# Kernel tuning notes

Measured on AMD Instinct MI355X. Metric: run time of the kernel, lower is better.

Reference implementation:

```python
import jax, jax.numpy as jnp
import numpy as np

EPS = 1e-5
NUM_HEADS = 16


def layernorm(x, g, b):
    m = jnp.mean(x, axis=-1, keepdims=True)
    v = jnp.mean(jnp.square(x - m), axis=-1, keepdims=True)
    return (x - m) * jax.lax.rsqrt(v + EPS) * g + b


def setup_inputs() -> dict:
    key = jax.random.key(0)
    ks = jax.random.split(key, 8)
    B, S, E, F = 16, 512, 1024, 4096
    s_e = 1.0 / np.sqrt(E)
    s_f = 1.0 / np.sqrt(F)
    return {
        "input": jax.random.normal(ks[0], (B, S, E), jnp.float32),
        "ln1_g": jnp.ones((E,), jnp.float32),
        "ln1_b": jnp.zeros((E,), jnp.float32),
        "wq": jax.random.normal(ks[1], (E, E), jnp.float32) * s_e,
        "bq": jnp.zeros((E,), jnp.float32),
        "wk": jax.random.normal(ks[2], (E, E), jnp.float32) * s_e,
        "bk": jnp.zeros((E,), jnp.float32),
        "wv": jax.random.normal(ks[3], (E, E), jnp.float32) * s_e,
        "bv": jnp.zeros((E,), jnp.float32),
        "wo": jax.random.normal(ks[4], (E, E), jnp.float32) * s_e,
        "bo": jnp.zeros((E,), jnp.float32),
        "ln2_g": jnp.ones((E,), jnp.float32),
        "ln2_b": jnp.zeros((E,), jnp.float32),
        "w1": jax.random.normal(ks[5], (E, F), jnp.float32) * s_e,
        "b1": jnp.zeros((F,), jnp.float32),
        "w2": jax.random.normal(ks[6], (F, E), jnp.float32) * s_f,
        "b2": jnp.zeros((E,), jnp.float32),
    }


def attention(x, wq, bq, wk, bk, wv, bv, wo, bo):
    B, S, E = x.shape
    H = NUM_HEADS
    D = E // H
    q = (x @ wq + bq).reshape(B, S, H, D)
    k = (x @ wk + bk).reshape(B, S, H, D)
    v = (x @ wv + bv).reshape(B, S, H, D)
    scores = jnp.einsum("bqhd,bkhd->bhqk", q, k) * (1.0 / np.sqrt(D))
    attn = jax.nn.softmax(scores, axis=-1)
    out = jnp.einsum("bhqk,bkhd->bqhd", attn, v).reshape(B, S, E)
    return out @ wo + bo


def reference(input, ln1_g, ln1_b, wq, bq, wk, bk, wv, bv, wo, bo,
              ln2_g, ln2_b, w1, b1, w2, b2):
    # pre-LN attention + residual
    x = layernorm(input, ln1_g, ln1_b)
    x = attention(x, wq, bq, wk, bk, wv, bv, wo, bo)
    x = x + input
    # pre-LN MLP (GELU exact, matching nn.GELU default) + residual
    y = layernorm(x, ln2_g, ln2_b)
    y = jax.nn.gelu(y @ w1 + b1, approximate=False)
    y = y @ w2 + b2
    return x + y
```

## Files before the change

### kernel.cpp

```cpp
#include <hip/hip_runtime.h>
#include <hip/hip_bf16.h>


typedef __bf16 bf16x8 __attribute__((ext_vector_type(8)));
typedef __bf16 bf16x4 __attribute__((ext_vector_type(4)));
typedef float  f32x4  __attribute__((ext_vector_type(4)));

#define EPI_QKV  0
#define EPI_RES  1
#define EPI_GELU 2

__device__ __forceinline__ void async_copy16(const void* g, void* l) {
  __builtin_amdgcn_global_load_lds((const __attribute__((address_space(1))) void*)g,
                                   (__attribute__((address_space(3))) void*)l, 16, 0, 0);
}

__global__ __launch_bounds__(256) void prep_weights(
    const float* __restrict__ wq, const float* __restrict__ wk,
    const float* __restrict__ wv, const float* __restrict__ wo,
    const float* __restrict__ w1, const float* __restrict__ w2,
    const float* __restrict__ bq, const float* __restrict__ bk,
    const float* __restrict__ bv,
    __bf16* __restrict__ wqkvT, __bf16* __restrict__ woT,
    __bf16* __restrict__ w1T, __bf16* __restrict__ w2T, float* __restrict__ bqkv) {
  const int bid = blockIdx.x;
  if (bid >= 12288) {
    const int i = (bid - 12288) * 256 + threadIdx.x;
    bqkv[i] = (i < 1024) ? bq[i] : ((i < 2048) ? bk[i - 1024] : bv[i - 2048]);
    return;
  }
  const float* in;
  __bf16* out;
  int K, N, tile;
  if (bid < 4096) {
    const int w = bid >> 10;
    tile = bid & 1023;
    in = (w == 0) ? wq : (w == 1) ? wk : (w == 2) ? wv : wo;
    out = (w == 3) ? woT : (wqkvT + (size_t)w * 1024 * 1024);
    K = 1024; N = 1024;
  } else if (bid < 8192) { tile = bid - 4096; in = w1; out = w1T; K = 1024; N = 4096; }
  else                   { tile = bid - 8192; in = w2; out = w2T; K = 4096; N = 1024; }
  const int ntx = N >> 5;
  const int bx = tile % ntx, by = tile / ntx;
  const int n0 = bx * 32, k0 = by * 32;

  __shared__ float tilebuf[32][33];
  const int tx = threadIdx.x & 31, ty = threadIdx.x >> 5;
#pragma unroll
  for (int i = 0; i < 4; i++)
    tilebuf[ty + i * 8][tx] = in[(size_t)(k0 + ty + i * 8) * N + n0 + tx];
  __syncthreads();
#pragma unroll
  for (int i = 0; i < 4; i++)
    out[(size_t)(n0 + ty + i * 8) * K + k0 + tx] = (__bf16)tilebuf[tx][ty + i * 8];
}

__device__ __forceinline__ float block_sum(float v, float* red) {
#pragma unroll
  for (int off = 32; off; off >>= 1) v += __shfl_down(v, off);
  const int w = threadIdx.x >> 6;
  __syncthreads();
  if ((threadIdx.x & 63) == 0) red[w] = v;
  __syncthreads();
  return red[0] + red[1] + red[2] + red[3];
}

__global__ __launch_bounds__(256) void ln_kernel(const float* __restrict__ x,
                                                 const float* __restrict__ g,
                                                 const float* __restrict__ bta,
                                                 __bf16* __restrict__ out) {
  __shared__ float red[8];
  const int row = blockIdx.x, t = threadIdx.x;
  const float4 v = ((const float4*)(x + (size_t)row * 1024))[t];
  float s = v.x + v.y + v.z + v.w;
  s = block_sum(s, red);
  const float mean = s * (1.0f / 1024.0f);
  const float d0 = v.x - mean, d1 = v.y - mean, d2 = v.z - mean, d3 = v.w - mean;
  float vs = d0 * d0 + d1 * d1 + d2 * d2 + d3 * d3;
  vs = block_sum(vs, red);
  const float rstd = rsqrtf(vs * (1.0f / 1024.0f) + 1e-5f);
  const float4 gg = ((const float4*)g)[t];
  const float4 bb = ((const float4*)bta)[t];
  bf16x4 o;
  o[0] = (__bf16)(d0 * rstd * gg.x + bb.x);
  o[1] = (__bf16)(d1 * rstd * gg.y + bb.y);
  o[2] = (__bf16)(d2 * rstd * gg.z + bb.z);
  o[3] = (__bf16)(d3 * rstd * gg.w + bb.w);
  ((bf16x4*)out)[(size_t)row * 256 + t] = o;
}

template <int EPI>
__global__ __launch_bounds__(256, 2) void gemm_bt(const __bf16* __restrict__ A,
                                                  const __bf16* __restrict__ Bt,
                                                  const float* __restrict__ bias,
                                                  const float* __restrict__ res,
                                                  void* __restrict__ out,
                                                  void* __restrict__ out2,
                                                  int N, int K) {
  __shared__ __bf16 lA[128 * 64];
  __shared__ __bf16 lB[128 * 64];
  const int t = threadIdx.x;
  const int wave = t >> 6, lane = t & 63;
  const int lm = lane & 15, lq = lane >> 4;

  const int Ntiles = gridDim.x;
  const int flat = blockIdx.y * Ntiles + blockIdx.x;
  const int xcd = flat & 7;
  const int local = flat >> 3;
  const int tn = local % Ntiles;
  const int tm = (local / Ntiles) * 8 + xcd;
  const int m0 = tm * 128, n0 = tn * 128;
  const int wm = (wave & 1) * 64, wn = (wave >> 1) * 64;

  f32x4 acc[4][4] = {};

  const int srow = t >> 3, sslot = t & 7;
  const int schunk = sslot ^ (srow & 7);
  const __bf16* aSrc = A + (size_t)(m0 + srow) * K + schunk * 8;
  const __bf16* bSrc = Bt + (size_t)(n0 + srow) * K + schunk * 8;

  for (int k0 = 0; k0 < K; k0 += 64) {
#pragma unroll
    for (int i = 0; i < 4; i++) {
      async_copy16(aSrc + (size_t)(i * 32) * K, lA + i * 2048 + t * 8);
      async_copy16(bSrc + (size_t)(i * 32) * K, lB + i * 2048 + t * 8);
    }
    aSrc += 64; bSrc += 64;
    __syncthreads();
#pragma unroll
    for (int kk = 0; kk < 2; kk++) {
      bf16x8 af[4], bf[4];
      const int slot = (kk * 4 + lq) ^ (lm & 7);
#pragma unroll
      for (int i = 0; i < 4; i++) {
        af[i] = *(const bf16x8*)&lA[(wm + i * 16 + lm) * 64 + slot * 8];
        bf[i] = *(const bf16x8*)&lB[(wn + i * 16 + lm) * 64 + slot * 8];
      }
#pragma unroll
      for (int mi = 0; mi < 4; mi++)
#pragma unroll
        for (int ni = 0; ni < 4; ni++)
          acc[mi][ni] = __builtin_amdgcn_mfma_f32_16x16x32_bf16(af[mi], bf[ni], acc[mi][ni], 0, 0, 0);
    }
    __syncthreads();
  }

#pragma unroll
  for (int mi = 0; mi < 4; mi++) {
    const int gr = m0 + wm + mi * 16 + lq * 4;
#pragma unroll
    for (int ni = 0; ni < 4; ni++) {
      const int gc = n0 + wn + ni * 16 + lm;
      const float bv = bias[gc];
#pragma unroll
      for (int r = 0; r < 4; r++) {
        float v = acc[mi][ni][r] + bv;
        const int row = gr + r;
        if (EPI == EPI_GELU) {
          v = 0.5f * v * (1.0f + erff(v * 0.70710678118654752f));
          ((__bf16*)out)[(size_t)row * N + gc] = (__bf16)v;
        } else if (EPI == EPI_RES) {
          ((float*)out)[(size_t)row * N + gc] = v + res[(size_t)row * N + gc];
        } else {
          if (gc < 2048) {
            ((__bf16*)out)[(size_t)row * 2048 + gc] = (__bf16)v;
          } else {
            const int d = gc & 63, hh = (gc - 2048) >> 6;
            const int bb = row >> 9, ss = row & 511;
            ((__bf16*)out2)[(((size_t)bb * 16 + hh) * 64 + d) * 512 + ss] = (__bf16)v;
          }
        }
      }
    }
  }
}

__global__ __launch_bounds__(256) void attn_kernel(const __bf16* __restrict__ qk,
                                                   const __bf16* __restrict__ Vt,
                                                   __bf16* __restrict__ outA) {
  __shared__ __bf16 lK[128 * 64];
  __shared__ __bf16 lV[64 * 128];
  __shared__ __bf16 lP[4][16 * 128];
  const int t = threadIdx.x, wave = t >> 6, lane = t & 63;
  const int lm = lane & 15, lq = lane >> 4;
  const int sw = lm & 7;
  const int flat = blockIdx.x;
  const int xcd = flat & 7, local = flat >> 3;
  const int qt = local & 7;
  const int bh = (local >> 3) * 8 + xcd;
  const int h = bh & 15, b = bh >> 4;
  const int q0 = qt * 64 + wave * 16;

  const size_t qrow = (size_t)(b * 512 + q0 + lm) * 2048 + h * 64;
  bf16x8 aq0 = *(const bf16x8*)&qk[qrow + lq * 8];
  bf16x8 aq1 = *(const bf16x8*)&qk[qrow + 32 + lq * 8];

  float mrow[4] = {-3e38f, -3e38f, -3e38f, -3e38f};
  float lrow[4] = {0.f, 0.f, 0.f, 0.f};
  f32x4 o[4] = {};

  const int krow = t >> 3;
  const int kchunk = (t & 7) ^ (krow & 7);
  const __bf16* kSrc = qk + (size_t)(b * 512 + krow) * 2048 + 1024 + h * 64 + kchunk * 8;
  const int vrow = t >> 4;
  const int vchunk = (t & 15) ^ (vrow & 7);
  const __bf16* vSrc = Vt + ((size_t)bh * 64 + vrow) * 512 + vchunk * 8;

  for (int kt = 0; kt < 4; kt++) {
#pragma unroll
    for (int i = 0; i < 4; i++) {
      async_copy16(kSrc + (size_t)(kt * 128 + i * 32) * 2048, lK + i * 2048 + t * 8);
      async_copy16(vSrc + kt * 128 + (size_t)(i * 16) * 512, lV + i * 2048 + t * 8);
    }
    __syncthreads();

    f32x4 s[8];
#pragma unroll
    for (int ni = 0; ni < 8; ni++) {
      bf16x8 bk0 = *(const bf16x8*)&lK[(ni * 16 + lm) * 64 + ((lq ^ sw) * 8)];
      bf16x8 bk1 = *(const bf16x8*)&lK[(ni * 16 + lm) * 64 + (((4 + lq) ^ sw) * 8)];
      f32x4 z = {};
      z = __builtin_amdgcn_mfma_f32_16x16x32_bf16(aq0, bk0, z, 0, 0, 0);
      z = __builtin_amdgcn_mfma_f32_16x16x32_bf16(aq1, bk1, z, 0, 0, 0);
      s[ni] = z;
    }
#pragma unroll
    for (int ni = 0; ni < 8; ni++)
#pragma unroll
      for (int r = 0; r < 4; r++) s[ni][r] *= 0.125f;

    float mnew[4], alpha[4];
#pragma unroll
    for (int r = 0; r < 4; r++) {
      float mx = s[0][r];
#pragma unroll
      for (int ni = 1; ni < 8; ni++) mx = fmaxf(mx, s[ni][r]);
#pragma unroll
      for (int off = 1; off < 16; off <<= 1) mx = fmaxf(mx, __shfl_xor(mx, off));
      mnew[r] = fmaxf(mrow[r], mx);
      alpha[r] = __expf(mrow[r] - mnew[r]);
      mrow[r] = mnew[r];
    }
    float rs[4] = {0.f, 0.f, 0.f, 0.f};
#pragma unroll
    for (int ni = 0; ni < 8; ni++)
#pragma unroll
      for (int r = 0; r < 4; r++) {
        const float p = __expf(s[ni][r] - mnew[r]);
        s[ni][r] = p;
        rs[r] += p;
      }
#pragma unroll
    for (int r = 0; r < 4; r++) {
#pragma unroll
      for (int off = 1; off < 16; off <<= 1) rs[r] += __shfl_xor(rs[r], off);
      lrow[r] = lrow[r] * alpha[r] + rs[r];
    }

#pragma unroll
    for (int ni = 0; ni < 8; ni++) {
      const int chunk = ni * 2 + (lm >> 3);
#pragma unroll
      for (int r = 0; r < 4; r++) {
        const int q = lq * 4 + r;
        lP[wave][q * 128 + ((chunk ^ (q & 7)) * 8) + (lm & 7)] = (__bf16)s[ni][r];
      }
    }
    asm volatile("s_waitcnt lgkmcnt(0)" ::: "memory");
    bf16x8 ap[4];
#pragma unroll
    for (int kc = 0; kc < 4; kc++)
      ap[kc] = *(const bf16x8*)&lP[wave][lm * 128 + (((kc * 4 + lq) ^ sw) * 8)];

#pragma unroll
    for (int di = 0; di < 4; di++)
#pragma unroll
      for (int r = 0; r < 4; r++) o[di][r] *= alpha[r];

#pragma unroll
    for (int di = 0; di < 4; di++) {
#pragma unroll
      for (int kc = 0; kc < 4; kc++) {
        bf16x8 bv = *(const bf16x8*)&lV[(di * 16 + lm) * 128 + (((kc * 4 + lq) ^ sw) * 8)];
        o[di] = __builtin_amdgcn_mfma_f32_16x16x32_bf16(ap[kc], bv, o[di], 0, 0, 0);
      }
    }
    __syncthreads();
  }

#pragma unroll
  for (int di = 0; di < 4; di++)
#pragma unroll
    for (int r = 0; r < 4; r++) {
      const float v = o[di][r] / lrow[r];
      outA[(size_t)(b * 512 + q0 + lq * 4 + r) * 1024 + h * 64 + di * 16 + lm] = (__bf16)v;
    }
}

extern "C" void kernel_launch(void* const* d_in, const int* in_sizes, int n_in,
                              void* d_out, int out_size, void* d_ws, size_t ws_size,
                              hipStream_t stream) {
  const float* input = (const float*)d_in[0];
  const float* ln1_g = (const float*)d_in[1];
  const float* ln1_b = (const float*)d_in[2];
  const float* wq = (const float*)d_in[3];
  const float* bq = (const float*)d_in[4];
  const float* wk = (const float*)d_in[5];
  const float* bk = (const float*)d_in[6];
  const float* wv = (const float*)d_in[7];
  const float* bv = (const float*)d_in[8];
  const float* wo = (const float*)d_in[9];
  const float* bo = (const float*)d_in[10];
  const float* ln2_g = (const float*)d_in[11];
  const float* ln2_b = (const float*)d_in[12];
  const float* w1 = (const float*)d_in[13];
  const float* b1 = (const float*)d_in[14];
  const float* w2 = (const float*)d_in[15];
  const float* b2 = (const float*)d_in[16];

  char* ws = (char*)d_ws;
  __bf16* wqkvT = (__bf16*)(ws + 0);
  __bf16* woT   = (__bf16*)(ws + ((size_t)6 << 20));
  __bf16* w1T   = (__bf16*)(ws + ((size_t)8 << 20));
  __bf16* w2T   = (__bf16*)(ws + ((size_t)16 << 20));
  __bf16* qkbuf = (__bf16*)(ws + ((size_t)24 << 20));
  __bf16* vtbuf = (__bf16*)(ws + ((size_t)56 << 20));
  __bf16* abuf  = (__bf16*)(ws + ((size_t)72 << 20));
  float*  xbuf  = (float*) (ws + ((size_t)24 << 20));
  __bf16* ylnbuf= (__bf16*)(ws + ((size_t)56 << 20));
  __bf16* hbuf  = (__bf16*)(ws + ((size_t)72 << 20));
  float*  bqkv  = (float*) (ws + ((size_t)136 << 20));

  const dim3 blk(256);
  prep_weights<<<12300, blk, 0, stream>>>(wq, wk, wv, wo, w1, w2, bq, bk, bv,
                                          wqkvT, woT, w1T, w2T, bqkv);

  ln_kernel<<<8192, blk, 0, stream>>>(input, ln1_g, ln1_b, abuf);
  gemm_bt<EPI_QKV><<<dim3(24, 64), blk, 0, stream>>>(abuf, wqkvT, bqkv, nullptr,
                                                     qkbuf, vtbuf, 3072, 1024);
  attn_kernel<<<2048, blk, 0, stream>>>(qkbuf, vtbuf, abuf);
  gemm_bt<EPI_RES><<<dim3(8, 64), blk, 0, stream>>>(abuf, woT, bo, input,
                                                    xbuf, nullptr, 1024, 1024);
  ln_kernel<<<8192, blk, 0, stream>>>(xbuf, ln2_g, ln2_b, ylnbuf);
  gemm_bt<EPI_GELU><<<dim3(32, 64), blk, 0, stream>>>(ylnbuf, w1T, b1, nullptr,
                                                      hbuf, nullptr, 4096, 1024);
  gemm_bt<EPI_RES><<<dim3(8, 64), blk, 0, stream>>>(hbuf, w2T, b2, xbuf,
                                                    d_out, nullptr, 1024, 4096);
}
```

Measured before the change: 484.1 us.

## Add 256x256-tile 8-wave GEMM with interleaved staging for QKV and FC1

Adds a new GEMM kernel using 512-thread blocks and 256x256 output tiles. It double-buffers LDS and splits each K-step into four MFMA quads, with asynchronous global-to-LDS loads interleaved between them and wave priority raised around the MFMAs. The QKV projection and the first MLP GEMM now use this kernel. The aim is more data reuse per tile and better overlap of loads with matrix math, at the cost of heavy register and LDS use (128 KB LDS, large accumulator arrays) and fewer blocks per grid.

```diff
diff --git a/kernel.cpp b/kernel.cpp
--- a/kernel.cpp
+++ b/kernel.cpp
@@ -175,6 +175,159 @@
   }
 }
 
+#define MFMA_QUAD(MI0)                                                         \
+  do {                                                                         \
+    _Pragma("unroll") for (int kk = 0; kk < 2; ++kk) {                         \
+      _Pragma("unroll") for (int ni = 0; ni < 4; ++ni) {                       \
+        acc[MI0][ni] = __builtin_amdgcn_mfma_f32_16x16x32_bf16(                \
+            af[MI0][kk], bf[ni][kk], acc[MI0][ni], 0, 0, 0);                   \
+        acc[(MI0) + 1][ni] = __builtin_amdgcn_mfma_f32_16x16x32_bf16(          \
+            af[(MI0) + 1][kk], bf[ni][kk], acc[(MI0) + 1][ni], 0, 0, 0);       \
+      }                                                                        \
+    }                                                                          \
+  } while (0)
+
+#define READ_A(MI)                                                             \
+  _Pragma("unroll") for (int kk = 0; kk < 2; ++kk)                             \
+      af[MI][kk] = *(const bf16x8*)&bufA[(wm * 128 + (MI)*16 + lm) * 64 +      \
+                                         (((kk * 4 + lq) ^ sw) * 8)];
+
+template <int EPI>
+__global__ __launch_bounds__(512, 2) void gemm8_bt(const __bf16* __restrict__ A,
+                                                   const __bf16* __restrict__ Bt,
+                                                   const float* __restrict__ bias,
+                                                   void* __restrict__ out,
+                                                   void* __restrict__ out2,
+                                                   int N, int K) {
+  __shared__ __bf16 lA[2 * 256 * 64];
+  __shared__ __bf16 lB[2 * 256 * 64];
+  const int t = threadIdx.x;
+  const int wave = t >> 6, lane = t & 63;
+  const int lm = lane & 15, lq = lane >> 4, sw = lm & 7;
+  const int wm = wave >> 2, wn = wave & 3;
+
+  const int Ntiles = gridDim.x;
+  const int flat = blockIdx.y * Ntiles + blockIdx.x;
+  const int xcd = flat & 7;
+  const int local = flat >> 3;
+  const int tn = local % Ntiles;
+  const int tm = (local / Ntiles) * 8 + xcd;
+  const int m0 = tm * 256, n0 = tn * 256;
+
+  const int NT = K >> 6;
+
+  const int srow = t >> 3;
+  const int schunk = (t & 7) ^ (srow & 7);
+  const __bf16* aBase = A + (size_t)(m0 + srow) * K + schunk * 8;
+  const __bf16* bBase = Bt + (size_t)(n0 + srow) * K + schunk * 8;
+  __bf16* ldA = lA + t * 8;
+  __bf16* ldB = lB + t * 8;
+
+  auto stage = [&](int h) {
+    if (h >= 4 * NT) return;
+    const int tau = h >> 2, type = h & 3, hf = type & 1;
+    const size_t roff = (size_t)(hf * 128) * K + (size_t)tau * 64;
+    const int loff = (tau & 1) * 16384 + hf * 8192;
+    if (type < 2) {
+      async_copy16(aBase + roff, ldA + loff);
+      async_copy16(aBase + roff + (size_t)64 * K, ldA + loff + 4096);
+    } else {
+      async_copy16(bBase + roff, ldB + loff);
+      async_copy16(bBase + roff + (size_t)64 * K, ldB + loff + 4096);
+    }
+  };
+
+  f32x4 acc[8][4] = {};
+
+  for (int h = 0; h < 6; ++h) stage(h);
+  asm volatile("s_waitcnt vmcnt(4)" ::: "memory");
+  __builtin_amdgcn_s_barrier();
+
+  for (int tt = 0; tt < NT; ++tt) {
+    const __bf16* bufA = lA + (tt & 1) * 16384;
+    const __bf16* bufB = lB + (tt & 1) * 16384;
+    bf16x8 af[8][2], bf[4][2];
+
+#pragma unroll
+    for (int ni = 0; ni < 4; ++ni)
+#pragma unroll
+      for (int kk = 0; kk < 2; ++kk)
+        bf[ni][kk] = *(const bf16x8*)&bufB[(wn * 64 + ni * 16 + lm) * 64 +
+                                           (((kk * 4 + lq) ^ sw) * 8)];
+    READ_A(0)
+    READ_A(1)
+    stage(4 * tt + 6);
+    __builtin_amdgcn_s_barrier();
+    asm volatile("s_waitcnt lgkmcnt(0)" ::: "memory");
+    __builtin_amdgcn_sched_barrier(0);
+    __builtin_amdgcn_s_setprio(1);
+    MFMA_QUAD(0);
+    __builtin_amdgcn_s_setprio(0);
+    __builtin_amdgcn_s_barrier();
+
+    READ_A(2)
+    READ_A(3)
+    READ_A(4)
+    READ_A(5)
+    READ_A(6)
+    READ_A(7)
+    stage(4 * tt + 7);
+    __builtin_amdgcn_s_barrier();
+    asm volatile("s_waitcnt lgkmcnt(0)" ::: "memory");
+    __builtin_amdgcn_sched_barrier(0);
+    __builtin_amdgcn_s_setprio(1);
+    MFMA_QUAD(2);
+    __builtin_amdgcn_s_setprio(0);
+    __builtin_amdgcn_s_barrier();
+
+    stage(4 * tt + 8);
+    __builtin_amdgcn_s_barrier();
+    __builtin_amdgcn_s_setprio(1);
+    MFMA_QUAD(4);
+    __builtin_amdgcn_s_setprio(0);
+    __builtin_amdgcn_s_barrier();
+
+    stage(4 * tt + 9);
+    __builtin_amdgcn_s_barrier();
+    __builtin_amdgcn_s_setprio(1);
+    MFMA_QUAD(6);
+    __builtin_amdgcn_s_setprio(0);
+
+    if (tt < NT - 1) {
+      if (tt == NT - 2) asm volatile("s_waitcnt vmcnt(0)" ::: "memory");
+      else              asm volatile("s_waitcnt vmcnt(4)" ::: "memory");
+      __builtin_amdgcn_s_barrier();
+    }
+  }
+
+#pragma unroll
+  for (int mi = 0; mi < 8; ++mi) {
+    const int gr = m0 + wm * 128 + mi * 16 + lq * 4;
+#pragma unroll
+    for (int ni = 0; ni < 4; ++ni) {
+      const int gc = n0 + wn * 64 + ni * 16 + lm;
+      const float bv = bias[gc];
+#pragma unroll
+      for (int r = 0; r < 4; ++r) {
+        float v = acc[mi][ni][r] + bv;
+        const int row = gr + r;
+        if (EPI == EPI_GELU) {
+          v = 0.5f * v * (1.0f + erff(v * 0.70710678118654752f));
+          ((__bf16*)out)[(size_t)row * N + gc] = (__bf16)v;
+        } else {
+          if (gc < 2048) {
+            ((__bf16*)out)[(size_t)row * 2048 + gc] = (__bf16)v;
+          } else {
+            const int d = gc & 63, hh = (gc - 2048) >> 6;
+            const int bb = row >> 9, ss = row & 511;
+            ((__bf16*)out2)[(((size_t)bb * 16 + hh) * 64 + d) * 512 + ss] = (__bf16)v;
+          }
+        }
+      }
+    }
+  }
+}
+
 __global__ __launch_bounds__(256) void attn_kernel(const __bf16* __restrict__ qk,
                                                    const __bf16* __restrict__ Vt,
                                                    __bf16* __restrict__ outA) {
@@ -332,18 +485,19 @@
   float*  bqkv  = (float*) (ws + ((size_t)136 << 20));
 
   const dim3 blk(256);
+  const dim3 blk8(512);
   prep_weights<<<12300, blk, 0, stream>>>(wq, wk, wv, wo, w1, w2, bq, bk, bv,
                                           wqkvT, woT, w1T, w2T, bqkv);
 
   ln_kernel<<<8192, blk, 0, stream>>>(input, ln1_g, ln1_b, abuf);
-  gemm_bt<EPI_QKV><<<dim3(24, 64), blk, 0, stream>>>(abuf, wqkvT, bqkv, nullptr,
-                                                     qkbuf, vtbuf, 3072, 1024);
+  gemm8_bt<EPI_QKV><<<dim3(12, 32), blk8, 0, stream>>>(abuf, wqkvT, bqkv,
+                                                       qkbuf, vtbuf, 3072, 1024);
   attn_kernel<<<2048, blk, 0, stream>>>(qkbuf, vtbuf, abuf);
   gemm_bt<EPI_RES><<<dim3(8, 64), blk, 0, stream>>>(abuf, woT, bo, input,
                                                     xbuf, nullptr, 1024, 1024);
   ln_kernel<<<8192, blk, 0, stream>>>(xbuf, ln2_g, ln2_b, ylnbuf);
-  gemm_bt<EPI_GELU><<<dim3(32, 64), blk, 0, stream>>>(ylnbuf, w1T, b1, nullptr,
-                                                      hbuf, nullptr, 4096, 1024);
+  gemm8_bt<EPI_GELU><<<dim3(16, 32), blk8, 0, stream>>>(ylnbuf, w1T, b1,
+                                                        hbuf, nullptr, 4096, 1024);
   gemm_bt<EPI_RES><<<dim3(8, 64), blk, 0, stream>>>(hbuf, w2T, b2, xbuf,
                                                     d_out, nullptr, 1024, 4096);
 }
```

Result: slower. 512.9 us (+6.0%).
